# Performance work log

Measured on AMD Instinct MI355X. Metric: run time of the kernel, lower is better.

## Reference

```python
import jax, jax.numpy as jnp
import numpy as np

RBF_DIM = 64          # args.radius_emb_dim
FOLD_DIM = 128        # args.fold_dim
PROT_RADIUS = 30.0    # args.protein_radius (GaussianSmearing stop)
NP_, NL_, E_ = 100000, 50000, 500000


def gaussian_smearing(d):
    # GaussianSmearing(start=0, stop=PROT_RADIUS, num_gaussians=RBF_DIM)
    offsets = jnp.linspace(0.0, PROT_RADIUS, RBF_DIM, dtype=d.dtype)  # [R]
    coeff = -0.5 / (offsets[1] - offsets[0]) ** 2
    return jnp.exp(coeff * (d[:, None] - offsets[None, :]) ** 2)  # [E, R]


def setup_inputs() -> dict:
    key = jax.random.key(0)
    ks = jax.random.split(key, 12)
    scale = 10.0  # spread positions so distances span [0, PROT_RADIUS]
    pos = lambda k, n: jax.random.normal(k, (n, 3), jnp.float32) * scale
    inp = {
        'lig_pos': pos(ks[0], NL_),
        'prot_pos': pos(ks[1], NP_),
        'prot_pos_Cb': pos(ks[2], NP_),
        'prot_pos_C': pos(ks[3], NP_),
        'prot_pos_O': pos(ks[4], NP_),
        'prot_pos_N': pos(ks[5], NP_),
        'W1': jax.random.normal(ks[6], (5 * RBF_DIM, FOLD_DIM), jnp.float32) * 0.05,
        'b1': jnp.zeros((FOLD_DIM,), jnp.float32),
        'W2': jax.random.normal(ks[7], (FOLD_DIM, FOLD_DIM), jnp.float32) * 0.05,
        'b2': jnp.zeros((FOLD_DIM,), jnp.float32),
        'src': jax.random.randint(ks[8], (E_,), 0, NL_, jnp.int32),   # ligand index per edge
        'dst': jax.random.randint(ks[9], (E_,), 0, NP_, jnp.int32),   # protein index per edge
    }
    return inp


def reference(lig_pos, prot_pos, prot_pos_Cb, prot_pos_C, prot_pos_O, prot_pos_N,
              W1, b1, W2, b2, src, dst):
    lp = lig_pos[src]  # [E, 3] gather of ligand positions
    # 5 distance channels: CA/Cb/C/O/N protein atoms, each RBF-smeared
    feats = [gaussian_smearing(jnp.linalg.norm(lp - p[dst], axis=-1))
             for p in (prot_pos, prot_pos_Cb, prot_pos_C, prot_pos_O, prot_pos_N)]
    edge_attr = jnp.concatenate(feats, axis=-1)  # [E, 5*RBF_DIM]
    h = jax.nn.relu(edge_attr @ W1 + b1)         # [E, FOLD_DIM]
    return h @ W2 + b2                           # [E, FOLD_DIM]
```

## Files before the change

### kernel.cpp

```cpp
#include <hip/hip_runtime.h>
#include <hip/hip_bf16.h>

typedef unsigned short ushort_t;
typedef unsigned int uint_t;
typedef __attribute__((ext_vector_type(8))) short short8;
typedef __attribute__((ext_vector_type(4))) float f32x4;
typedef __attribute__((ext_vector_type(2))) uint_t uint2_t;

#define FOLD 128
#define S_CONST 1.78357580f
#define DS_CONST 0.84932180f

__device__ __forceinline__ uint_t pkbf(float a, float b) {
    __hip_bfloat162 h2 = __float22bfloat162_rn(float2{a, b});
    uint_t u;
    __builtin_memcpy(&u, &h2, sizeof(u));
    return u;
}

__global__ __launch_bounds__(256) void pack_pos(
    const float* __restrict__ p0, const float* __restrict__ p1,
    const float* __restrict__ p2, const float* __restrict__ p3,
    const float* __restrict__ p4, const float* __restrict__ lig,
    float* __restrict__ P5, float* __restrict__ L4, int NP, int NL)
{
    int i = blockIdx.x * 256 + threadIdx.x;
    if (i < NP) {
        float r[16];
        const float* ps0 = p0 + 3 * i; const float* ps1 = p1 + 3 * i;
        const float* ps2 = p2 + 3 * i; const float* ps3 = p3 + 3 * i;
        const float* ps4 = p4 + 3 * i;
        r[0]=ps0[0]; r[1]=ps0[1]; r[2]=ps0[2];
        r[3]=ps1[0]; r[4]=ps1[1]; r[5]=ps1[2];
        r[6]=ps2[0]; r[7]=ps2[1]; r[8]=ps2[2];
        r[9]=ps3[0]; r[10]=ps3[1]; r[11]=ps3[2];
        r[12]=ps4[0]; r[13]=ps4[1]; r[14]=ps4[2];
        r[15]=0.f;
        #pragma unroll
        for (int k = 0; k < 4; ++k)
            *reinterpret_cast<f32x4*>(&P5[(size_t)i * 16 + k * 4]) =
                *reinterpret_cast<f32x4*>(&r[k * 4]);
    } else if (i < NP + NL) {
        int j = i - NP;
        f32x4 v = {lig[3 * j], lig[3 * j + 1], lig[3 * j + 2], 0.f};
        *reinterpret_cast<f32x4*>(&L4[(size_t)j * 4]) = v;
    }
}

#define NWAVES 8
#define W1_OFF 0
#define W2_OFF 20480
#define B1_OFF 28672
#define B2_OFF 28800
#define H_OFF  28928
#define LDS_DW 37120

template<bool PACKED>
__global__ __launch_bounds__(512) void fused(
    const float* __restrict__ lig,
    const float* __restrict__ p0, const float* __restrict__ p1,
    const float* __restrict__ p2, const float* __restrict__ p3,
    const float* __restrict__ p4,
    const float* __restrict__ P5, const float* __restrict__ L4,
    const float* __restrict__ W1, const float* __restrict__ W2,
    const float* __restrict__ b1, const float* __restrict__ b2,
    const int* __restrict__ src, const int* __restrict__ dst,
    float* __restrict__ out, int E)
{
    extern __shared__ uint_t smem[];
    uint_t* W1L = smem + W1_OFF;
    uint_t* W2L = smem + W2_OFF;
    const float* b1L = (const float*)(smem + B1_OFF);
    const float* b2L = (const float*)(smem + B2_OFF);

    const int t = threadIdx.x;
    const int w = t >> 6;
    const int l = t & 63;
    const int eL = l & 15, g = l >> 4;
    uint_t* hw = smem + H_OFF + (w << 10);

    for (int idx = t; idx < 20480; idx += 512) {
        int jj = idx & 3, l2 = (idx >> 2) & 63, nt = (idx >> 8) & 7, ks = idx >> 11;
        int row = ks * 32 + ((l2 >> 4) << 3) + 2 * jj;
        int col = nt * 16 + (l2 & 15);
        W1L[idx] = pkbf(W1[row * FOLD + col], W1[(row + 1) * FOLD + col]);
    }
    for (int idx = t; idx < 8192; idx += 512) {
        int jj = idx & 3, l2 = (idx >> 2) & 63, nt = (idx >> 8) & 7, ks = idx >> 11;
        int row = ks * 32 + ((l2 >> 4) << 3) + 2 * jj;
        int col = nt * 16 + (l2 & 15);
        W2L[idx] = pkbf(W2[row * FOLD + col], W2[(row + 1) * FOLD + col]);
    }
    if (t < 128) ((float*)(smem + B1_OFF))[t] = b1[t];
    else if (t < 256) ((float*)(smem + B2_OFF))[t - 128] = b2[t - 128];
    __syncthreads();

    const int NT = (E + 31) >> 5;
    const int stride = gridDim.x * NWAVES;
    int wt = blockIdx.x * NWAVES + w;
    if (wt >= NT) return;

    const float* GP = (g == 0) ? p0 : (g == 1) ? p1 : (g == 2) ? p2 : p3;
    const float* GPp = PACKED ? (P5 + g * 3) : nullptr;
    const bool g0 = (g == 0);
    const float gbase = (float)(8 * g) * DS_CONST;

    float Ax[2], Ay[2], Az[2], Px[2], Py[2], Pz[2], Qx[2], Qy[2], Qz[2];
    #pragma unroll
    for (int eh = 0; eh < 2; ++eh) {
        int e = wt * 32 + eh * 16 + eL; if (e >= E) e = E - 1;
        int s = src[e], d2 = dst[e];
        if constexpr (PACKED) {
            f32x4 lv = *reinterpret_cast<const f32x4*>(&L4[(size_t)s * 4]);
            Ax[eh] = lv[0]; Ay[eh] = lv[1]; Az[eh] = lv[2];
            const float* rp = GPp + (size_t)d2 * 16;
            Px[eh] = rp[0]; Py[eh] = rp[1]; Pz[eh] = rp[2];
            if (g0) {
                const float* qp = P5 + (size_t)d2 * 16 + 12;
                Qx[eh] = qp[0]; Qy[eh] = qp[1]; Qz[eh] = qp[2];
            }
        } else {
            Ax[eh] = lig[3 * s]; Ay[eh] = lig[3 * s + 1]; Az[eh] = lig[3 * s + 2];
            Px[eh] = GP[3 * d2]; Py[eh] = GP[3 * d2 + 1]; Pz[eh] = GP[3 * d2 + 2];
            if (g0) { Qx[eh] = p4[3 * d2]; Qy[eh] = p4[3 * d2 + 1]; Qz[eh] = p4[3 * d2 + 2]; }
        }
    }
    int sB[2], dB[2];
    if (wt + stride < NT) {
        #pragma unroll
        for (int eh = 0; eh < 2; ++eh) {
            int e = (wt + stride) * 32 + eh * 16 + eL; if (e >= E) e = E - 1;
            sB[eh] = src[e]; dB[eh] = dst[e];
        }
    }

    while (true) {
        const int wt2 = wt + stride;
        const bool more = (wt2 < NT);

        float Bx[2], By[2], Bz[2], Rx[2], Ry[2], Rz[2], Sx[2], Sy[2], Sz[2];
        if (more) {
            #pragma unroll
            for (int eh = 0; eh < 2; ++eh) {
                if constexpr (PACKED) {
                    f32x4 lv = *reinterpret_cast<const f32x4*>(&L4[(size_t)sB[eh] * 4]);
                    Bx[eh] = lv[0]; By[eh] = lv[1]; Bz[eh] = lv[2];
                    const float* rp = GPp + (size_t)dB[eh] * 16;
                    Rx[eh] = rp[0]; Ry[eh] = rp[1]; Rz[eh] = rp[2];
                    if (g0) {
                        const float* qp = P5 + (size_t)dB[eh] * 16 + 12;
                        Sx[eh] = qp[0]; Sy[eh] = qp[1]; Sz[eh] = qp[2];
                    }
                } else {
                    Bx[eh] = lig[3 * sB[eh]]; By[eh] = lig[3 * sB[eh] + 1]; Bz[eh] = lig[3 * sB[eh] + 2];
                    Rx[eh] = GP[3 * dB[eh]]; Ry[eh] = GP[3 * dB[eh] + 1]; Rz[eh] = GP[3 * dB[eh] + 2];
                    if (g0) { Sx[eh] = p4[3 * dB[eh]]; Sy[eh] = p4[3 * dB[eh] + 1]; Sz[eh] = p4[3 * dB[eh] + 2]; }
                }
            }
        }
        int sB2[2], dB2[2];
        if (wt2 + stride < NT) {
            #pragma unroll
            for (int eh = 0; eh < 2; ++eh) {
                int e = (wt2 + stride) * 32 + eh * 16 + eL; if (e >= E) e = E - 1;
                sB2[eh] = src[e]; dB2[eh] = dst[e];
            }
        }

        float u00[5][2];
        #pragma unroll
        for (int eh = 0; eh < 2; ++eh) {
            float dx = Ax[eh] - Px[eh], dy = Ay[eh] - Py[eh], dz = Az[eh] - Pz[eh];
            float dm = sqrtf(dx * dx + dy * dy + dz * dz);
            float d4 = 0.f;
            if (g0) {
                float ex = Ax[eh] - Qx[eh], ey = Ay[eh] - Qy[eh], ez = Az[eh] - Qz[eh];
                d4 = sqrtf(ex * ex + ey * ey + ez * ez);
            }
            #pragma unroll
            for (int c = 0; c < 4; ++c)
                u00[c][eh] = __builtin_fmaf(__shfl(dm, c * 16 + eL), S_CONST, -gbase);
            u00[4][eh] = __builtin_fmaf(__shfl(d4, eL), S_CONST, -gbase);
        }

        short8 a[2][10];
        #pragma unroll
        for (int ks = 0; ks < 10; ++ks) {
            const int c = ks >> 1;
            #pragma unroll
            for (int eh = 0; eh < 2; ++eh) {
                uint_t dwv[4];
                #pragma unroll
                for (int jj = 0; jj < 4; ++jj) {
                    float k0 = (float)((ks & 1) * 32 + 2 * jj) * DS_CONST;
                    float k1 = (float)((ks & 1) * 32 + 2 * jj + 1) * DS_CONST;
                    float ua = u00[c][eh] - k0;
                    float ub = u00[c][eh] - k1;
                    float va = __builtin_amdgcn_exp2f(-(ua * ua));
                    float vb = __builtin_amdgcn_exp2f(-(ub * ub));
                    dwv[jj] = pkbf(va, vb);
                }
                __builtin_memcpy(&a[eh][ks], dwv, 16);
            }
        }

        f32x4 acc1[8][2];
        #pragma unroll
        for (int nt = 0; nt < 8; ++nt)
            #pragma unroll
            for (int eh = 0; eh < 2; ++eh) acc1[nt][eh] = f32x4{0.f, 0.f, 0.f, 0.f};
        #pragma unroll
        for (int ks = 0; ks < 10; ++ks) {
            #pragma unroll
            for (int nt = 0; nt < 8; ++nt) {
                const short8 wf = *reinterpret_cast<const short8*>(&W1L[((ks * 8 + nt) * 64 + l) * 4]);
                acc1[nt][0] = __builtin_amdgcn_mfma_f32_16x16x32_bf16(wf, a[0][ks], acc1[nt][0], 0, 0, 0);
                acc1[nt][1] = __builtin_amdgcn_mfma_f32_16x16x32_bf16(wf, a[1][ks], acc1[nt][1], 0, 0, 0);
            }
        }

        const int swzE = (eL & 7) << 3;
        #pragma unroll
        for (int eh = 0; eh < 2; ++eh) {
            #pragma unroll
            for (int nt = 0; nt < 8; ++nt) {
                f32x4 bv = *reinterpret_cast<const f32x4*>(&b1L[nt * 16 + g * 4]);
                float v0 = fmaxf(acc1[nt][eh][0] + bv[0], 0.f);
                float v1 = fmaxf(acc1[nt][eh][1] + bv[1], 0.f);
                float v2 = fmaxf(acc1[nt][eh][2] + bv[2], 0.f);
                float v3 = fmaxf(acc1[nt][eh][3] + bv[3], 0.f);
                uint2_t pv;
                pv[0] = pkbf(v0, v1);
                pv[1] = pkbf(v2, v3);
                *reinterpret_cast<uint2_t*>(&hw[eL * 64 + ((nt * 8 + g * 2) ^ swzE)]) = pv;
            }
            f32x4 acc2[8];
            #pragma unroll
            for (int nt = 0; nt < 8; ++nt) acc2[nt] = f32x4{0.f, 0.f, 0.f, 0.f};
            #pragma unroll
            for (int ks2 = 0; ks2 < 4; ++ks2) {
                const short8 hf = *reinterpret_cast<const short8*>(&hw[eL * 64 + ((ks2 * 16 + g * 4) ^ swzE)]);
                #pragma unroll
                for (int nt = 0; nt < 8; ++nt) {
                    const short8 wf2 = *reinterpret_cast<const short8*>(&W2L[((ks2 * 8 + nt) * 64 + l) * 4]);
                    acc2[nt] = __builtin_amdgcn_mfma_f32_16x16x32_bf16(wf2, hf, acc2[nt], 0, 0, 0);
                }
            }
            int e = wt * 32 + eh * 16 + eL;
            if (e < E) {
                #pragma unroll
                for (int nt = 0; nt < 8; ++nt) {
                    f32x4 bv2 = *reinterpret_cast<const f32x4*>(&b2L[nt * 16 + g * 4]);
                    f32x4 v = acc2[nt] + bv2;
                    __builtin_nontemporal_store(v,
                        reinterpret_cast<f32x4*>(&out[(size_t)e * FOLD + nt * 16 + g * 4]));
                }
            }
            asm volatile("s_waitcnt lgkmcnt(0)" ::: "memory");
        }

        if (!more) break;
        wt = wt2;
        #pragma unroll
        for (int eh = 0; eh < 2; ++eh) {
            Ax[eh] = Bx[eh]; Ay[eh] = By[eh]; Az[eh] = Bz[eh];
            Px[eh] = Rx[eh]; Py[eh] = Ry[eh]; Pz[eh] = Rz[eh];
            if (g0) { Qx[eh] = Sx[eh]; Qy[eh] = Sy[eh]; Qz[eh] = Sz[eh]; }
            sB[eh] = sB2[eh]; dB[eh] = dB2[eh];
        }
    }
}

extern "C" void kernel_launch(void* const* d_in, const int* in_sizes, int n_in,
                              void* d_out, int out_size, void* d_ws, size_t ws_size,
                              hipStream_t stream) {
    const float* lig = (const float*)d_in[0];
    const float* p0  = (const float*)d_in[1];
    const float* p1  = (const float*)d_in[2];
    const float* p2  = (const float*)d_in[3];
    const float* p3  = (const float*)d_in[4];
    const float* p4  = (const float*)d_in[5];
    const float* W1  = (const float*)d_in[6];
    const float* b1  = (const float*)d_in[7];
    const float* W2  = (const float*)d_in[8];
    const float* b2  = (const float*)d_in[9];
    const int* src   = (const int*)d_in[10];
    const int* dst   = (const int*)d_in[11];
    float* out = (float*)d_out;
    const int E  = in_sizes[10];
    const int NL = in_sizes[0] / 3;
    const int NP = in_sizes[1] / 3;

    const size_t need = ((size_t)NP * 16 + (size_t)NL * 4) * sizeof(float);
    const bool packed = (ws_size >= need);

    hipFuncSetAttribute(reinterpret_cast<const void*>(fused<true>),
                        hipFuncAttributeMaxDynamicSharedMemorySize, LDS_DW * 4);
    hipFuncSetAttribute(reinterpret_cast<const void*>(fused<false>),
                        hipFuncAttributeMaxDynamicSharedMemorySize, LDS_DW * 4);

    if (packed) {
        float* P5 = (float*)d_ws;
        float* L4 = P5 + (size_t)NP * 16;
        pack_pos<<<(NP + NL + 255) / 256, 256, 0, stream>>>(p0, p1, p2, p3, p4, lig,
                                                            P5, L4, NP, NL);
        fused<true><<<256, 512, LDS_DW * 4, stream>>>(lig, p0, p1, p2, p3, p4, P5, L4,
                                                      W1, W2, b1, b2, src, dst, out, E);
    } else {
        fused<false><<<256, 512, LDS_DW * 4, stream>>>(lig, p0, p1, p2, p3, p4,
                                                       nullptr, nullptr,
                                                       W1, W2, b1, b2, src, dst, out, E);
    }
}
```

Before: 115.1 us.

## Split distance computation into a separate gather kernel before the MLP kernel

Adds a kernel that gathers ligand and packed protein positions per edge and writes the five distances to a workspace buffer. The main MFMA kernel then reads these distances with contiguous loads instead of doing indirect gathers and sqrt, so its loop should be simpler and use fewer registers. In exchange it adds a kernel launch and an extra write and read of five floats per edge through global memory, and it needs a larger workspace. The old fused gather path is kept as a fallback.

```diff
diff --git a/kernel.cpp b/kernel.cpp
--- a/kernel.cpp
+++ b/kernel.cpp
@@ -47,6 +47,33 @@
     }
 }
 
+__global__ __launch_bounds__(256) void dist_k(
+    const float* __restrict__ P5, const float* __restrict__ L4,
+    const int* __restrict__ src, const int* __restrict__ dst,
+    float* __restrict__ D, int E)
+{
+    int e = blockIdx.x * 256 + threadIdx.x;
+    if (e >= E) return;
+    int s = src[e], d2 = dst[e];
+    f32x4 lv = *reinterpret_cast<const f32x4*>(&L4[(size_t)s * 4]);
+    f32x4 r0 = *reinterpret_cast<const f32x4*>(&P5[(size_t)d2 * 16]);
+    f32x4 r1 = *reinterpret_cast<const f32x4*>(&P5[(size_t)d2 * 16 + 4]);
+    f32x4 r2 = *reinterpret_cast<const f32x4*>(&P5[(size_t)d2 * 16 + 8]);
+    f32x4 r3 = *reinterpret_cast<const f32x4*>(&P5[(size_t)d2 * 16 + 12]);
+    float px[5] = {r0[0], r0[3], r1[2], r2[1], r3[0]};
+    float py[5] = {r0[1], r1[0], r1[3], r2[2], r3[1]};
+    float pz[5] = {r0[2], r1[1], r2[0], r2[3], r3[2]};
+    float dv[5];
+    #pragma unroll
+    for (int c = 0; c < 5; ++c) {
+        float dx = lv[0] - px[c], dy = lv[1] - py[c], dz = lv[2] - pz[c];
+        dv[c] = sqrtf(dx * dx + dy * dy + dz * dz);
+    }
+    f32x4 v4 = {dv[0], dv[1], dv[2], dv[3]};
+    *reinterpret_cast<f32x4*>(&D[(size_t)e * 5]) = v4;
+    D[(size_t)e * 5 + 4] = dv[4];
+}
+
 #define NWAVES 8
 #define W1_OFF 0
 #define W2_OFF 20480
@@ -55,13 +82,166 @@
 #define H_OFF  28928
 #define LDS_DW 37120
 
-template<bool PACKED>
-__global__ __launch_bounds__(512) void fused(
+__global__ __launch_bounds__(512) void fused_d(
+    const float* __restrict__ D,
+    const float* __restrict__ W1, const float* __restrict__ W2,
+    const float* __restrict__ b1, const float* __restrict__ b2,
+    float* __restrict__ out, int E)
+{
+    extern __shared__ uint_t smem[];
+    uint_t* W1L = smem + W1_OFF;
+    uint_t* W2L = smem + W2_OFF;
+    const float* b1L = (const float*)(smem + B1_OFF);
+    const float* b2L = (const float*)(smem + B2_OFF);
+
+    const int t = threadIdx.x;
+    const int w = t >> 6;
+    const int l = t & 63;
+    const int eL = l & 15, g = l >> 4;
+    uint_t* hw = smem + H_OFF + (w << 10);
+
+    for (int idx = t; idx < 20480; idx += 512) {
+        int jj = idx & 3, l2 = (idx >> 2) & 63, nt = (idx >> 8) & 7, ks = idx >> 11;
+        int row = ks * 32 + ((l2 >> 4) << 3) + 2 * jj;
+        int col = nt * 16 + (l2 & 15);
+        W1L[idx] = pkbf(W1[row * FOLD + col], W1[(row + 1) * FOLD + col]);
+    }
+    for (int idx = t; idx < 8192; idx += 512) {
+        int jj = idx & 3, l2 = (idx >> 2) & 63, nt = (idx >> 8) & 7, ks = idx >> 11;
+        int row = ks * 32 + ((l2 >> 4) << 3) + 2 * jj;
+        int col = nt * 16 + (l2 & 15);
+        W2L[idx] = pkbf(W2[row * FOLD + col], W2[(row + 1) * FOLD + col]);
+    }
+    if (t < 128) ((float*)(smem + B1_OFF))[t] = b1[t];
+    else if (t < 256) ((float*)(smem + B2_OFF))[t - 128] = b2[t - 128];
+    __syncthreads();
+
+    const int NT = (E + 31) >> 5;
+    const int stride = gridDim.x * NWAVES;
+    int wt = blockIdx.x * NWAVES + w;
+    if (wt >= NT) return;
+
+    const float gbase = (float)(8 * g) * DS_CONST;
+
+    f32x4 d03[2]; float d4v[2];
+    #pragma unroll
+    for (int eh = 0; eh < 2; ++eh) {
+        int e = wt * 32 + eh * 16 + eL; if (e >= E) e = E - 1;
+        d03[eh] = *reinterpret_cast<const f32x4*>(&D[(size_t)e * 5]);
+        d4v[eh] = D[(size_t)e * 5 + 4];
+    }
+
+    while (true) {
+        const int wt2 = wt + stride;
+        const bool more = (wt2 < NT);
+
+        f32x4 nd03[2]; float nd4[2];
+        if (more) {
+            #pragma unroll
+            for (int eh = 0; eh < 2; ++eh) {
+                int e = wt2 * 32 + eh * 16 + eL; if (e >= E) e = E - 1;
+                nd03[eh] = *reinterpret_cast<const f32x4*>(&D[(size_t)e * 5]);
+                nd4[eh] = D[(size_t)e * 5 + 4];
+            }
+        }
+
+        float u00[5][2];
+        #pragma unroll
+        for (int eh = 0; eh < 2; ++eh) {
+            #pragma unroll
+            for (int c = 0; c < 4; ++c)
+                u00[c][eh] = __builtin_fmaf(d03[eh][c], S_CONST, -gbase);
+            u00[4][eh] = __builtin_fmaf(d4v[eh], S_CONST, -gbase);
+        }
+
+        short8 a[2][10];
+        #pragma unroll
+        for (int ks = 0; ks < 10; ++ks) {
+            const int c = ks >> 1;
+            #pragma unroll
+            for (int eh = 0; eh < 2; ++eh) {
+                uint_t dwv[4];
+                #pragma unroll
+                for (int jj = 0; jj < 4; ++jj) {
+                    float k0 = (float)((ks & 1) * 32 + 2 * jj) * DS_CONST;
+                    float k1 = (float)((ks & 1) * 32 + 2 * jj + 1) * DS_CONST;
+                    float ua = u00[c][eh] - k0;
+                    float ub = u00[c][eh] - k1;
+                    float va = __builtin_amdgcn_exp2f(-(ua * ua));
+                    float vb = __builtin_amdgcn_exp2f(-(ub * ub));
+                    dwv[jj] = pkbf(va, vb);
+                }
+                __builtin_memcpy(&a[eh][ks], dwv, 16);
+            }
+        }
+
+        f32x4 acc1[8][2];
+        #pragma unroll
+        for (int nt = 0; nt < 8; ++nt)
+            #pragma unroll
+            for (int eh = 0; eh < 2; ++eh) acc1[nt][eh] = f32x4{0.f, 0.f, 0.f, 0.f};
+        #pragma unroll
+        for (int ks = 0; ks < 10; ++ks) {
+            #pragma unroll
+            for (int nt = 0; nt < 8; ++nt) {
+                const short8 wf = *reinterpret_cast<const short8*>(&W1L[((ks * 8 + nt) * 64 + l) * 4]);
+                acc1[nt][0] = __builtin_amdgcn_mfma_f32_16x16x32_bf16(wf, a[0][ks], acc1[nt][0], 0, 0, 0);
+                acc1[nt][1] = __builtin_amdgcn_mfma_f32_16x16x32_bf16(wf, a[1][ks], acc1[nt][1], 0, 0, 0);
+            }
+        }
+
+        const int swzE = (eL & 7) << 3;
+        #pragma unroll
+        for (int eh = 0; eh < 2; ++eh) {
+            #pragma unroll
+            for (int nt = 0; nt < 8; ++nt) {
+                f32x4 bv = *reinterpret_cast<const f32x4*>(&b1L[nt * 16 + g * 4]);
+                float v0 = fmaxf(acc1[nt][eh][0] + bv[0], 0.f);
+                float v1 = fmaxf(acc1[nt][eh][1] + bv[1], 0.f);
+                float v2 = fmaxf(acc1[nt][eh][2] + bv[2], 0.f);
+                float v3 = fmaxf(acc1[nt][eh][3] + bv[3], 0.f);
+                uint2_t pv;
+                pv[0] = pkbf(v0, v1);
+                pv[1] = pkbf(v2, v3);
+                *reinterpret_cast<uint2_t*>(&hw[eL * 64 + ((nt * 8 + g * 2) ^ swzE)]) = pv;
+            }
+            f32x4 acc2[8];
+            #pragma unroll
+            for (int nt = 0; nt < 8; ++nt) acc2[nt] = f32x4{0.f, 0.f, 0.f, 0.f};
+            #pragma unroll
+            for (int ks2 = 0; ks2 < 4; ++ks2) {
+                const short8 hf = *reinterpret_cast<const short8*>(&hw[eL * 64 + ((ks2 * 16 + g * 4) ^ swzE)]);
+                #pragma unroll
+                for (int nt = 0; nt < 8; ++nt) {
+                    const short8 wf2 = *reinterpret_cast<const short8*>(&W2L[((ks2 * 8 + nt) * 64 + l) * 4]);
+                    acc2[nt] = __builtin_amdgcn_mfma_f32_16x16x32_bf16(wf2, hf, acc2[nt], 0, 0, 0);
+                }
+            }
+            int e = wt * 32 + eh * 16 + eL;
+            if (e < E) {
+                #pragma unroll
+                for (int nt = 0; nt < 8; ++nt) {
+                    f32x4 bv2 = *reinterpret_cast<const f32x4*>(&b2L[nt * 16 + g * 4]);
+                    f32x4 v = acc2[nt] + bv2;
+                    __builtin_nontemporal_store(v,
+                        reinterpret_cast<f32x4*>(&out[(size_t)e * FOLD + nt * 16 + g * 4]));
+                }
+            }
+            asm volatile("s_waitcnt lgkmcnt(0)" ::: "memory");
+        }
+
+        if (!more) break;
+        wt = wt2;
+        #pragma unroll
+        for (int eh = 0; eh < 2; ++eh) { d03[eh] = nd03[eh]; d4v[eh] = nd4[eh]; }
+    }
+}
+
+__global__ __launch_bounds__(512) void fused_g(
     const float* __restrict__ lig,
     const float* __restrict__ p0, const float* __restrict__ p1,
     const float* __restrict__ p2, const float* __restrict__ p3,
     const float* __restrict__ p4,
-    const float* __restrict__ P5, const float* __restrict__ L4,
     const float* __restrict__ W1, const float* __restrict__ W2,
     const float* __restrict__ b1, const float* __restrict__ b2,
     const int* __restrict__ src, const int* __restrict__ dst,
@@ -101,7 +281,6 @@
     if (wt >= NT) return;
 
     const float* GP = (g == 0) ? p0 : (g == 1) ? p1 : (g == 2) ? p2 : p3;
-    const float* GPp = PACKED ? (P5 + g * 3) : nullptr;
     const bool g0 = (g == 0);
     const float gbase = (float)(8 * g) * DS_CONST;
 
@@ -110,20 +289,9 @@
     for (int eh = 0; eh < 2; ++eh) {
         int e = wt * 32 + eh * 16 + eL; if (e >= E) e = E - 1;
         int s = src[e], d2 = dst[e];
-        if constexpr (PACKED) {
-            f32x4 lv = *reinterpret_cast<const f32x4*>(&L4[(size_t)s * 4]);
-            Ax[eh] = lv[0]; Ay[eh] = lv[1]; Az[eh] = lv[2];
-            const float* rp = GPp + (size_t)d2 * 16;
-            Px[eh] = rp[0]; Py[eh] = rp[1]; Pz[eh] = rp[2];
-            if (g0) {
-                const float* qp = P5 + (size_t)d2 * 16 + 12;
-                Qx[eh] = qp[0]; Qy[eh] = qp[1]; Qz[eh] = qp[2];
-            }
-        } else {
-            Ax[eh] = lig[3 * s]; Ay[eh] = lig[3 * s + 1]; Az[eh] = lig[3 * s + 2];
-            Px[eh] = GP[3 * d2]; Py[eh] = GP[3 * d2 + 1]; Pz[eh] = GP[3 * d2 + 2];
-            if (g0) { Qx[eh] = p4[3 * d2]; Qy[eh] = p4[3 * d2 + 1]; Qz[eh] = p4[3 * d2 + 2]; }
-        }
+        Ax[eh] = lig[3 * s]; Ay[eh] = lig[3 * s + 1]; Az[eh] = lig[3 * s + 2];
+        Px[eh] = GP[3 * d2]; Py[eh] = GP[3 * d2 + 1]; Pz[eh] = GP[3 * d2 + 2];
+        if (g0) { Qx[eh] = p4[3 * d2]; Qy[eh] = p4[3 * d2 + 1]; Qz[eh] = p4[3 * d2 + 2]; }
     }
     int sB[2], dB[2];
     if (wt + stride < NT) {
@@ -142,20 +310,9 @@
         if (more) {
             #pragma unroll
             for (int eh = 0; eh < 2; ++eh) {
-                if constexpr (PACKED) {
-                    f32x4 lv = *reinterpret_cast<const f32x4*>(&L4[(size_t)sB[eh] * 4]);
-                    Bx[eh] = lv[0]; By[eh] = lv[1]; Bz[eh] = lv[2];
-                    const float* rp = GPp + (size_t)dB[eh] * 16;
-                    Rx[eh] = rp[0]; Ry[eh] = rp[1]; Rz[eh] = rp[2];
-                    if (g0) {
-                        const float* qp = P5 + (size_t)dB[eh] * 16 + 12;
-                        Sx[eh] = qp[0]; Sy[eh] = qp[1]; Sz[eh] = qp[2];
-                    }
-                } else {
-                    Bx[eh] = lig[3 * sB[eh]]; By[eh] = lig[3 * sB[eh] + 1]; Bz[eh] = lig[3 * sB[eh] + 2];
-                    Rx[eh] = GP[3 * dB[eh]]; Ry[eh] = GP[3 * dB[eh] + 1]; Rz[eh] = GP[3 * dB[eh] + 2];
-                    if (g0) { Sx[eh] = p4[3 * dB[eh]]; Sy[eh] = p4[3 * dB[eh] + 1]; Sz[eh] = p4[3 * dB[eh] + 2]; }
-                }
+                Bx[eh] = lig[3 * sB[eh]]; By[eh] = lig[3 * sB[eh] + 1]; Bz[eh] = lig[3 * sB[eh] + 2];
+                Rx[eh] = GP[3 * dB[eh]]; Ry[eh] = GP[3 * dB[eh] + 1]; Rz[eh] = GP[3 * dB[eh] + 2];
+                if (g0) { Sx[eh] = p4[3 * dB[eh]]; Sy[eh] = p4[3 * dB[eh] + 1]; Sz[eh] = p4[3 * dB[eh] + 2]; }
             }
         }
         int sB2[2], dB2[2];
@@ -291,24 +448,23 @@
     const int NL = in_sizes[0] / 3;
     const int NP = in_sizes[1] / 3;
 
-    const size_t need = ((size_t)NP * 16 + (size_t)NL * 4) * sizeof(float);
-    const bool packed = (ws_size >= need);
-
-    hipFuncSetAttribute(reinterpret_cast<const void*>(fused<true>),
+    const size_t need = ((size_t)NP * 16 + (size_t)NL * 4 + (size_t)E * 5) * sizeof(float);
+
+    hipFuncSetAttribute(reinterpret_cast<const void*>(fused_d),
                         hipFuncAttributeMaxDynamicSharedMemorySize, LDS_DW * 4);
-    hipFuncSetAttribute(reinterpret_cast<const void*>(fused<false>),
+    hipFuncSetAttribute(reinterpret_cast<const void*>(fused_g),
                         hipFuncAttributeMaxDynamicSharedMemorySize, LDS_DW * 4);
 
-    if (packed) {
+    if (ws_size >= need) {
         float* P5 = (float*)d_ws;
         float* L4 = P5 + (size_t)NP * 16;
+        float* D  = L4 + (size_t)NL * 4;
         pack_pos<<<(NP + NL + 255) / 256, 256, 0, stream>>>(p0, p1, p2, p3, p4, lig,
                                                             P5, L4, NP, NL);
-        fused<true><<<256, 512, LDS_DW * 4, stream>>>(lig, p0, p1, p2, p3, p4, P5, L4,
-                                                      W1, W2, b1, b2, src, dst, out, E);
+        dist_k<<<(E + 255) / 256, 256, 0, stream>>>(P5, L4, src, dst, D, E);
+        fused_d<<<256, 512, LDS_DW * 4, stream>>>(D, W1, W2, b1, b2, out, E);
     } else {
-        fused<false><<<256, 512, LDS_DW * 4, stream>>>(lig, p0, p1, p2, p3, p4,
-                                                       nullptr, nullptr,
-                                                       W1, W2, b1, b2, src, dst, out, E);
-    }
-}
+        fused_g<<<256, 512, LDS_DW * 4, stream>>>(lig, p0, p1, p2, p3, p4,
+                                                  W1, W2, b1, b2, src, dst, out, E);
+    }
+}
```

New measurement: 117.1 us. No clear change (+1.7%).
